# Kernel tuning notes

Hardware: AMD Instinct MI355X
Metric: run time of the kernel (lower is better)

Reference implementation:

```python
import jax, jax.numpy as jnp
import numpy as np
from jax import lax

FILTER_SIZE = 11
SIGMA = 1.5
K1, K2 = 0.01, 0.03
WEIGHTS = jnp.array([0.0448, 0.2856, 0.3001, 0.2363, 0.1333], dtype=jnp.float32)


def _gauss_1d(size, sigma):
    coords = jnp.arange(size, dtype=jnp.float32) - (size - 1) / 2.0
    return jax.nn.softmax(-coords ** 2 / (2.0 * sigma ** 2))


def _gaussian_filter(x, k1d):
    # separable depthwise blur, VALID padding: horizontal then vertical
    C = x.shape[1]
    size = k1d.shape[0]
    kw = jnp.broadcast_to(k1d.reshape(1, 1, 1, size), (C, 1, 1, size))  # OIHW
    kh = jnp.broadcast_to(k1d.reshape(1, 1, size, 1), (C, 1, size, 1))
    dn = ('NCHW', 'OIHW', 'NCHW')
    x = lax.conv_general_dilated(x, kw, (1, 1), 'VALID', dimension_numbers=dn, feature_group_count=C)
    x = lax.conv_general_dilated(x, kh, (1, 1), 'VALID', dimension_numbers=dn, feature_group_count=C)
    return x


def _ssim(x, y, k1d, max_val):
    c1 = (K1 * max_val) ** 2
    c2 = (K2 * max_val) ** 2
    mu1 = _gaussian_filter(x, k1d)
    mu2 = _gaussian_filter(y, k1d)
    mu1_sq, mu2_sq, mu1_mu2 = mu1 ** 2, mu2 ** 2, mu1 * mu2
    sigma1_sq = _gaussian_filter(x * x, k1d) - mu1_sq
    sigma2_sq = _gaussian_filter(y * y, k1d) - mu2_sq
    sigma12 = _gaussian_filter(x * y, k1d) - mu1_mu2
    cs_map = (2 * sigma12 + c2) / (sigma1_sq + sigma2_sq + c2)
    ssim_map = (2 * mu1_mu2 + c1) / (mu1_sq + mu2_sq + c1) * cs_map
    return ssim_map.mean(axis=(-1, -2, -3)), cs_map.mean(axis=(-1, -2, -3))


def _avg_pool2(x):
    # torch avg_pool2d(kernel=2, padding=(H%2, W%2)), count_include_pad=True
    ph, pw = x.shape[-2] % 2, x.shape[-1] % 2
    if ph or pw:
        x = jnp.pad(x, ((0, 0), (0, 0), (ph, ph), (pw, pw)))
    N, C, H, W = x.shape
    return x.reshape(N, C, H // 2, 2, W // 2, 2).mean(axis=(-3, -1))


def setup_inputs() -> dict:
    key = jax.random.key(0)
    k1, k2 = jax.random.split(key)
    shape = (32, 3, 512, 512)
    return {
        'input': jax.random.uniform(k1, shape, dtype=jnp.float32),
        'target': jax.random.uniform(k2, shape, dtype=jnp.float32),
    }


def reference(input, target):
    k1d = _gauss_1d(FILTER_SIZE, SIGMA)
    max_val = target.max() - target.min()  # module default: max_val=None
    levels = WEIGHTS.shape[0]
    x, y = input, target
    mcs = []
    ssim_val = None
    for _ in range(levels):
        ssim_val, cs = _ssim(x, y, k1d, max_val)
        mcs.append(cs)
        x = _avg_pool2(x)
        y = _avg_pool2(y)
    mcs = jnp.stack(mcs, axis=0)  # (levels, N)
    # faithful to original: ssim_val ** w[-1] broadcast inside the product
    ms = jnp.prod(mcs[:-1] ** WEIGHTS[:-1, None] * ssim_val ** WEIGHTS[-1], axis=0)
    return ms.mean()
```

## Files before the change

kernel.cpp:

```cpp
#include <hip/hip_runtime.h>
#include <cmath>

#define FILT 11

typedef float v2f __attribute__((ext_vector_type(2)));

struct GW { float w[FILT]; };

__device__ __forceinline__ unsigned enc_f(float f) {
    unsigned u = __float_as_uint(f);
    return (u & 0x80000000u) ? ~u : (u | 0x80000000u);
}
__device__ __forceinline__ float dec_f(unsigned u) {
    return (u & 0x80000000u) ? __uint_as_float(u & 0x7FFFFFFFu)
                             : __uint_as_float(~u);
}

__global__ void init_acc(unsigned* ws) {
    int t = threadIdx.x;
    if (t == 0) { ws[0] = 0u; ws[1] = 0xFFFFFFFFu; }
    for (int i = 2 + t; i < 512; i += blockDim.x) ws[i] = 0u;
}

__global__ void minmax_kernel(const float4* __restrict__ t, long n4, unsigned* mm) {
    unsigned mx = 0u, mn = 0xFFFFFFFFu;
    long stride = (long)gridDim.x * blockDim.x;
    for (long i = (long)blockIdx.x * blockDim.x + threadIdx.x; i < n4; i += stride) {
        float4 v = t[i];
        unsigned a = enc_f(v.x), b = enc_f(v.y), c = enc_f(v.z), d = enc_f(v.w);
        mx = max(mx, max(max(a, b), max(c, d)));
        mn = min(mn, min(min(a, b), min(c, d)));
    }
    for (int off = 32; off; off >>= 1) {
        mx = max(mx, (unsigned)__shfl_down((int)mx, off));
        mn = min(mn, (unsigned)__shfl_down((int)mn, off));
    }
    __shared__ unsigned smx[4], smn[4];
    int wid = threadIdx.x >> 6, lane = threadIdx.x & 63;
    if (lane == 0) { smx[wid] = mx; smn[wid] = mn; }
    __syncthreads();
    if (threadIdx.x == 0) {
        for (int i = 1; i < 4; i++) { mx = max(mx, smx[i]); mn = min(mn, smn[i]); }
        atomicMax(&mm[0], mx);
        atomicMin(&mm[1], mn);
    }
}

__global__ __launch_bounds__(256) void ssim_stream(
    const float* __restrict__ x, const float* __restrict__ y,
    int H, int W, int NC, int nstrips, int nb, int B,
    const unsigned* __restrict__ mm,
    float* __restrict__ cs_sum, float* __restrict__ ssim_sum, GW gw,
    float* __restrict__ poolx, float* __restrict__ pooly, int do_pool)
{
    __shared__ v2f ring[4][2][80];

    const int wv = threadIdx.x >> 6;
    const int lane = threadIdx.x & 63;
    const int wid = blockIdx.x * 4 + wv;
    const int total = NC * nstrips * nb;
    if (wid >= total) return;

    const int band = wid % nb;
    const int t1 = wid / nb;
    const int strip = t1 % nstrips;
    const int img = t1 / nstrips;
    const int n = img / 3;

    const int Ho = H - (FILT - 1);
    const int Wo = W - (FILT - 1);
    const int a = band * B;
    if (a >= Ho) return;
    const int out_hi = min(a + B, Ho);
    const int bEnd = out_hi + (FILT - 1);

    const int base = strip * 64;
    const float* xp = x + (size_t)img * H * W;
    const float* yp = y + (size_t)img * H * W;
    const int c0 = min(base + lane, W - 1);
    const int c1 = min(base + 64 + min(lane, 9), W - 1);
    const bool colv = (base + lane) < Wo;

    const float mv = dec_f(mm[0]) - dec_f(mm[1]);
    const float c1c = (0.01f * mv) * (0.01f * mv);
    const float c2c = (0.03f * mv) * (0.03f * mv);

    const int Wp = W >> 1;
    size_t orow = (size_t)img * (H >> 1) * Wp + (size_t)(a >> 1) * Wp;
    const int pc = (base >> 1) + lane;
    const bool poolv = (lane < 32) && (pc < Wp);

    v2f* bufE = &ring[wv][0][0];
    v2f* bufO = &ring[wv][1][0];

    v2f acc01[FILT], acc23[FILT];
    float acc4[FILT];
#pragma unroll
    for (int s = 0; s < FILT; s++) {
        acc01[s] = (v2f){0.f, 0.f};
        acc23[s] = (v2f){0.f, 0.f};
        acc4[s] = 0.f;
    }

    float lcs = 0.f, lss = 0.f;

    float ex0, ey0, ex1, ey1, ox0, oy0, ox1, oy1;
    {
        const float* xe = xp + (size_t)a * W;
        const float* ye = yp + (size_t)a * W;
        ex0 = xe[c0]; ey0 = ye[c0]; ex1 = xe[c1]; ey1 = ye[c1];
        ox0 = xe[W + c0]; oy0 = ye[W + c0];
        ox1 = xe[W + c1]; oy1 = ye[W + c1];
    }
    const float* xe = xp + (size_t)(a + 2) * W;
    const float* ye = yp + (size_t)(a + 2) * W;
    const float* xo = xp + (size_t)(a + 3) * W;
    const float* yo = yp + (size_t)(a + 3) * W;

#pragma unroll 1
    for (int r0 = a; r0 < bEnd; r0 += 22) {
#pragma unroll
        for (int p = 0; p < FILT; p++) {
            const int r = r0 + 2 * p;
            if (r < bEnd) {
                const bool hasO = (r + 1 < bEnd);
                const int pe = (2 * p) % FILT;
                const int po = (2 * p + 1) % FILT;

                bufE[lane] = (v2f){ex0, ey0};
                if (lane < 10) bufE[64 + lane] = (v2f){ex1, ey1};
                if (hasO) {
                    bufO[lane] = (v2f){ox0, oy0};
                    if (lane < 10) bufO[64 + lane] = (v2f){ox1, oy1};
                }

                ex0 = xe[c0]; ey0 = ye[c0]; ex1 = xe[c1]; ey1 = ye[c1];
                ox0 = xo[c0]; oy0 = yo[c0]; ox1 = xo[c1]; oy1 = yo[c1];
                {
                    const int adv = (r + 4 < bEnd) ? 2 * W : 0;
                    xe += adv; ye += adv; xo += adv; yo += adv;
                }

                if (do_pool && hasO && poolv) {
                    float4 qe = *(const float4*)&bufE[2 * lane];
                    float4 qo = *(const float4*)&bufO[2 * lane];
                    poolx[orow + pc] = 0.25f * (qe.x + qe.z + qo.x + qo.z);
                    pooly[orow + pc] = 0.25f * (qe.y + qe.w + qo.y + qo.w);
                }
                orow += Wp;

                v2f h01e = (v2f){0.f, 0.f}, h23e = (v2f){0.f, 0.f};
                float h4e = 0.f;
#pragma unroll
                for (int k = 0; k < FILT; k++) {
                    v2f v = bufE[lane + k];
                    float w = gw.w[k];
                    v2f w2 = {w, w};
                    h01e = __builtin_elementwise_fma(w2, v, h01e);
                    v2f sq = v * v;
                    h23e = __builtin_elementwise_fma(w2, sq, h23e);
                    h4e = __builtin_fmaf(w, v.x * v.y, h4e);
                }
#pragma unroll
                for (int k = 0; k < FILT; k++) {
                    const int s = (pe - k + FILT) % FILT;
                    float w = gw.w[k];
                    v2f w2 = {w, w};
                    acc01[s] = __builtin_elementwise_fma(w2, h01e, acc01[s]);
                    acc23[s] = __builtin_elementwise_fma(w2, h23e, acc23[s]);
                    acc4[s] = __builtin_fmaf(w, h4e, acc4[s]);
                }
                const int eE = (pe + 1) % FILT;
                if (r >= a + (FILT - 1) && colv) {
                    float m1 = acc01[eE].x, m2 = acc01[eE].y;
                    float mu11 = m1 * m1, mu22 = m2 * m2, mu12 = m1 * m2;
                    float s1 = acc23[eE].x - mu11;
                    float s2 = acc23[eE].y - mu22;
                    float s12 = acc4[eE] - mu12;
                    float A = 2.f * s12 + c2c, Bv = s1 + s2 + c2c;
                    float Cv = 2.f * mu12 + c1c, Dv = mu11 + mu22 + c1c;
                    float r_ = __builtin_amdgcn_rcpf(Bv * Dv);
                    lcs += A * Dv * r_;
                    lss += Cv * A * r_;
                }
                acc01[eE] = (v2f){0.f, 0.f};
                acc23[eE] = (v2f){0.f, 0.f};
                acc4[eE] = 0.f;

                if (hasO) {
                    v2f h01o = (v2f){0.f, 0.f}, h23o = (v2f){0.f, 0.f};
                    float h4o = 0.f;
#pragma unroll
                    for (int k = 0; k < FILT; k++) {
                        v2f v = bufO[lane + k];
                        float w = gw.w[k];
                        v2f w2 = {w, w};
                        h01o = __builtin_elementwise_fma(w2, v, h01o);
                        v2f sq = v * v;
                        h23o = __builtin_elementwise_fma(w2, sq, h23o);
                        h4o = __builtin_fmaf(w, v.x * v.y, h4o);
                    }
#pragma unroll
                    for (int k = 0; k < FILT; k++) {
                        const int s = (po - k + FILT) % FILT;
                        float w = gw.w[k];
                        v2f w2 = {w, w};
                        acc01[s] = __builtin_elementwise_fma(w2, h01o, acc01[s]);
                        acc23[s] = __builtin_elementwise_fma(w2, h23o, acc23[s]);
                        acc4[s] = __builtin_fmaf(w, h4o, acc4[s]);
                    }
                    const int eO = (po + 1) % FILT;
                    if (r >= a + (FILT - 1) && colv) {
                        float m1 = acc01[eO].x, m2 = acc01[eO].y;
                        float mu11 = m1 * m1, mu22 = m2 * m2, mu12 = m1 * m2;
                        float s1 = acc23[eO].x - mu11;
                        float s2 = acc23[eO].y - mu22;
                        float s12 = acc4[eO] - mu12;
                        float A = 2.f * s12 + c2c, Bv = s1 + s2 + c2c;
                        float Cv = 2.f * mu12 + c1c, Dv = mu11 + mu22 + c1c;
                        float r_ = __builtin_amdgcn_rcpf(Bv * Dv);
                        lcs += A * Dv * r_;
                        lss += Cv * A * r_;
                    }
                    acc01[eO] = (v2f){0.f, 0.f};
                    acc23[eO] = (v2f){0.f, 0.f};
                    acc4[eO] = 0.f;
                }
            }
        }
    }

    for (int off = 32; off; off >>= 1) {
        lcs += __shfl_down(lcs, off);
        lss += __shfl_down(lss, off);
    }
    if (lane == 0) {
        atomicAdd(&cs_sum[n], lcs);
        atomicAdd(&ssim_sum[n], lss);
    }
}

__device__ __forceinline__ void ssim_lds_strip(
    const v2f* tile, int Wt, int Wo, int a, int out_hi, int lane,
    float c1c, float c2c, const GW& gw, float& lcs, float& lss)
{
    const int bEnd = out_hi + (FILT - 1);
    const int tl = min(lane, Wo - 1);
    const bool colv = lane < Wo;

    v2f acc01[FILT], acc23[FILT];
    float acc4[FILT];
#pragma unroll
    for (int s = 0; s < FILT; s++) {
        acc01[s] = (v2f){0.f, 0.f};
        acc23[s] = (v2f){0.f, 0.f};
        acc4[s] = 0.f;
    }

#pragma unroll 1
    for (int r0 = a; r0 < bEnd; r0 += FILT) {
#pragma unroll
        for (int p = 0; p < FILT; p++) {
            const int r = r0 + p;
            if (r < bEnd) {
                const v2f* row = tile + (size_t)r * Wt;
                v2f h01 = (v2f){0.f, 0.f}, h23 = (v2f){0.f, 0.f};
                float h4 = 0.f;
#pragma unroll
                for (int k = 0; k < FILT; k++) {
                    v2f v = row[tl + k];
                    float w = gw.w[k];
                    v2f w2 = {w, w};
                    h01 = __builtin_elementwise_fma(w2, v, h01);
                    v2f sq = v * v;
                    h23 = __builtin_elementwise_fma(w2, sq, h23);
                    h4 = __builtin_fmaf(w, v.x * v.y, h4);
                }
#pragma unroll
                for (int k = 0; k < FILT; k++) {
                    const int s = (p - k + FILT) % FILT;
                    float w = gw.w[k];
                    v2f w2 = {w, w};
                    acc01[s] = __builtin_elementwise_fma(w2, h01, acc01[s]);
                    acc23[s] = __builtin_elementwise_fma(w2, h23, acc23[s]);
                    acc4[s] = __builtin_fmaf(w, h4, acc4[s]);
                }
                const int e = (p + 1) % FILT;
                if (r >= a + (FILT - 1) && colv) {
                    float m1 = acc01[e].x, m2 = acc01[e].y;
                    float mu11 = m1 * m1, mu22 = m2 * m2, mu12 = m1 * m2;
                    float s1 = acc23[e].x - mu11;
                    float s2 = acc23[e].y - mu22;
                    float s12 = acc4[e] - mu12;
                    float A = 2.f * s12 + c2c, Bv = s1 + s2 + c2c;
                    float Cv = 2.f * mu12 + c1c, Dv = mu11 + mu22 + c1c;
                    float r_ = __builtin_amdgcn_rcpf(Bv * Dv);
                    lcs += A * Dv * r_;
                    lss += Cv * A * r_;
                }
                acc01[e] = (v2f){0.f, 0.f};
                acc23[e] = (v2f){0.f, 0.f};
                acc4[e] = 0.f;
            }
        }
    }
}

__global__ __launch_bounds__(1024) void ssim_tail(
    const float* __restrict__ x2, const float* __restrict__ y2,
    const unsigned* __restrict__ mm, float* __restrict__ ws2, GW gw,
    float* __restrict__ outp)
{
    __shared__ v2f ring[16][2][80];
    __shared__ v2f buf3[64 * 64];
    __shared__ v2f buf4[32 * 32];
    __shared__ int isLast;

    const int img = blockIdx.x;
    const int n = img / 3;
    const int wv = threadIdx.x >> 6;
    const int lane = threadIdx.x & 63;

    float* cs2 = ws2 + 2 + 2 * 32;
    float* cs3 = ws2 + 2 + 3 * 32;
    float* cs4 = ws2 + 2 + 4 * 32;
    float* ss2 = ws2 + 2 + 5 * 32 + 2 * 32;
    float* ss3 = ws2 + 2 + 5 * 32 + 3 * 32;
    float* ss4 = ws2 + 2 + 5 * 32 + 4 * 32;

    const float mv = dec_f(mm[0]) - dec_f(mm[1]);
    const float c1c = (0.01f * mv) * (0.01f * mv);
    const float c2c = (0.03f * mv) * (0.03f * mv);

    {
        const int strip = wv >> 3;
        const int band = wv & 7;
        const int H = 128, W = 128, Ho = 118, B = 16;
        const int a = band * B;
        const int out_hi = min(a + B, Ho);
        const int bEnd = out_hi + (FILT - 1);
        const int base = strip * 64;
        const float* xp = x2 + (size_t)img * H * W;
        const float* yp = y2 + (size_t)img * H * W;
        const int c0 = min(base + lane, W - 1);
        const int c1 = min(base + 64 + min(lane, 9), W - 1);
        const bool colv = (base + lane) < Ho;

        v2f* bufA = &ring[wv][0][0];
        v2f* bufB = &ring[wv][1][0];

        v2f acc01[FILT], acc23[FILT];
        float acc4[FILT];
#pragma unroll
        for (int s = 0; s < FILT; s++) {
            acc01[s] = (v2f){0.f, 0.f};
            acc23[s] = (v2f){0.f, 0.f};
            acc4[s] = 0.f;
        }
        float lcs = 0.f, lss = 0.f;

        const float* xr = xp + (size_t)a * W;
        const float* yr = yp + (size_t)a * W;
        float pfx0 = xr[c0], pfy0 = yr[c0];
        float pfx1 = xr[c1], pfy1 = yr[c1];

#pragma unroll 1
        for (int r0 = a; r0 < bEnd; r0 += FILT) {
#pragma unroll
            for (int p = 0; p < FILT; p++) {
                const int r = r0 + p;
                if (r < bEnd) {
                    v2f* bufc = (r & 1) ? bufB : bufA;
                    v2f* bufo = (r & 1) ? bufA : bufB;

                    bufc[lane] = (v2f){pfx0, pfy0};
                    if (lane < 10) bufc[64 + lane] = (v2f){pfx1, pfy1};

                    {
                        const int rn = min(r + 1, bEnd - 1);
                        const float* xn = xp + (size_t)rn * W;
                        const float* yn = yp + (size_t)rn * W;
                        pfx0 = xn[c0]; pfy0 = yn[c0];
                        pfx1 = xn[c1]; pfy1 = yn[c1];
                    }

                    v2f h01 = (v2f){0.f, 0.f}, h23 = (v2f){0.f, 0.f};
                    float h4 = 0.f;
#pragma unroll
                    for (int k = 0; k < FILT; k++) {
                        v2f v = bufc[lane + k];
                        float w = gw.w[k];
                        v2f w2 = {w, w};
                        h01 = __builtin_elementwise_fma(w2, v, h01);
                        v2f sq = v * v;
                        h23 = __builtin_elementwise_fma(w2, sq, h23);
                        h4 = __builtin_fmaf(w, v.x * v.y, h4);
                    }
#pragma unroll
                    for (int k = 0; k < FILT; k++) {
                        const int s = (p - k + FILT) % FILT;
                        float w = gw.w[k];
                        v2f w2 = {w, w};
                        acc01[s] = __builtin_elementwise_fma(w2, h01, acc01[s]);
                        acc23[s] = __builtin_elementwise_fma(w2, h23, acc23[s]);
                        acc4[s] = __builtin_fmaf(w, h4, acc4[s]);
                    }
                    const int e = (p + 1) % FILT;
                    if (r >= a + (FILT - 1) && colv) {
                        float m1 = acc01[e].x, m2 = acc01[e].y;
                        float mu11 = m1 * m1, mu22 = m2 * m2, mu12 = m1 * m2;
                        float s1 = acc23[e].x - mu11;
                        float s2 = acc23[e].y - mu22;
                        float s12 = acc4[e] - mu12;
                        float A = 2.f * s12 + c2c, Bv = s1 + s2 + c2c;
                        float Cv = 2.f * mu12 + c1c, Dv = mu11 + mu22 + c1c;
                        float r_ = __builtin_amdgcn_rcpf(Bv * Dv);
                        lcs += A * Dv * r_;
                        lss += Cv * A * r_;
                    }
                    acc01[e] = (v2f){0.f, 0.f};
                    acc23[e] = (v2f){0.f, 0.f};
                    acc4[e] = 0.f;

                    if ((r & 1) && r > a && lane < 32) {
                        const int pc = (base >> 1) + lane;
                        const int pr = r >> 1;
                        v2f q00 = bufo[2 * lane];
                        v2f q01 = bufo[2 * lane + 1];
                        v2f q10 = bufc[2 * lane];
                        v2f q11 = bufc[2 * lane + 1];
                        buf3[pr * 64 + pc] =
                            (q00 + q01 + q10 + q11) * (v2f){0.25f, 0.25f};
                    }
                }
            }
        }

        for (int off = 32; off; off >>= 1) {
            lcs += __shfl_down(lcs, off);
            lss += __shfl_down(lss, off);
        }
        if (lane == 0) {
            atomicAdd(&cs2[n], lcs);
            atomicAdd(&ss2[n], lss);
        }
    }
    __syncthreads();

    {
        const int pr = threadIdx.x >> 5;
        const int pc = threadIdx.x & 31;
        v2f q = (buf3[(2 * pr) * 64 + 2 * pc] + buf3[(2 * pr) * 64 + 2 * pc + 1] +
                 buf3[(2 * pr + 1) * 64 + 2 * pc] + buf3[(2 * pr + 1) * 64 + 2 * pc + 1]) *
                (v2f){0.25f, 0.25f};
        buf4[pr * 32 + pc] = q;
    }
    __syncthreads();

    {
        float lcs = 0.f, lss = 0.f;
        bool isL3 = (wv < 14);
        if (isL3) {
            const int a = wv * 4;
            ssim_lds_strip(buf3, 64, 54, a, min(a + 4, 54), lane,
                           c1c, c2c, gw, lcs, lss);
        } else {
            const int a = (wv - 14) * 12;
            ssim_lds_strip(buf4, 32, 22, a, min(a + 12, 22), lane,
                           c1c, c2c, gw, lcs, lss);
        }
        for (int off = 32; off; off >>= 1) {
            lcs += __shfl_down(lcs, off);
            lss += __shfl_down(lss, off);
        }
        if (lane == 0) {
            atomicAdd(isL3 ? &cs3[n] : &cs4[n], lcs);
            atomicAdd(isL3 ? &ss3[n] : &ss4[n], lss);
        }
    }

    __syncthreads();
    __threadfence();
    if (threadIdx.x == 0) {
        int old = atomicAdd((int*)(ws2 + 500), 1);
        isLast = (old == (int)gridDim.x - 1);
    }
    __syncthreads();
    if (isLast && threadIdx.x < 64) {
        const float cnt[5] = {3.f * 502 * 502, 3.f * 246 * 246, 3.f * 118 * 118,
                              3.f * 54 * 54, 3.f * 22 * 22};
        const float wts[5] = {0.0448f, 0.2856f, 0.3001f, 0.2363f, 0.1333f};
        int nn = threadIdx.x;
        float ms = 0.f;
        if (nn < 32) {
            float* cs = ws2 + 2;
            float* ss = ws2 + 2 + 5 * 32;
            float ssim = atomicAdd(&ss[4 * 32 + nn], 0.f) / cnt[4];
            float t = powf(ssim, wts[4]);
            ms = 1.f;
            for (int l = 0; l < 4; l++) {
                float cv = atomicAdd(&cs[l * 32 + nn], 0.f) / cnt[l];
                ms *= powf(cv, wts[l]) * t;
            }
        }
        for (int off = 32; off; off >>= 1) ms += __shfl_down(ms, off);
        if (threadIdx.x == 0) outp[0] = ms / 32.f;
    }
}

extern "C" void kernel_launch(void* const* d_in, const int* in_sizes, int n_in,
                              void* d_out, int out_size, void* d_ws, size_t ws_size,
                              hipStream_t stream) {
    const float* x0 = (const float*)d_in[0];
    const float* y0 = (const float*)d_in[1];
    float* out = (float*)d_out;
    float* ws = (float*)d_ws;
    unsigned* mm = (unsigned*)d_ws;
    float* cs_sum = ws + 2;
    float* ssim_sum = ws + 2 + 5 * 32;

    const int N = 32, C = 3, NC = N * C;

    float* wp = ws + 512;
    float* pxw1 = wp; wp += (size_t)NC * 256 * 256;
    float* pyw1 = wp; wp += (size_t)NC * 256 * 256;
    float* pxw2 = wp; wp += (size_t)NC * 128 * 128;
    float* pyw2 = wp; wp += (size_t)NC * 128 * 128;

    GW gw;
    {
        double tmp[FILT], s = 0.0;
        for (int k = 0; k < FILT; k++) {
            double c = (double)k - (FILT - 1) / 2.0;
            tmp[k] = exp(-c * c / (2.0 * 1.5 * 1.5));
            s += tmp[k];
        }
        for (int k = 0; k < FILT; k++) gw.w[k] = (float)(tmp[k] / s);
    }

    init_acc<<<1, 256, 0, stream>>>(mm);
    long n4 = (long)NC * 512 * 512 / 4;
    minmax_kernel<<<2048, 256, 0, stream>>>((const float4*)y0, n4, mm);

    {
        int H = 512, Ho = 502, nstrips = 8, B = 64;
        int nb = (Ho + B - 1) / B;
        int total = NC * nstrips * nb;
        int grid = (total + 3) / 4;
        ssim_stream<<<grid, 256, 0, stream>>>(
            x0, y0, H, H, NC, nstrips, nb, B, mm,
            cs_sum + 0 * 32, ssim_sum + 0 * 32, gw, pxw1, pyw1, 1);
    }
    {
        int H = 256, Ho = 246, nstrips = 4, B = 32;
        int nb = (Ho + B - 1) / B;
        int total = NC * nstrips * nb;
        int grid = (total + 3) / 4;
        ssim_stream<<<grid, 256, 0, stream>>>(
            pxw1, pyw1, H, H, NC, nstrips, nb, B, mm,
            cs_sum + 1 * 32, ssim_sum + 1 * 32, gw, pxw2, pyw2, 1);
    }
    ssim_tail<<<NC, 1024, 0, stream>>>(pxw2, pyw2, mm, ws, gw, out);
}
```

Baseline: 322.0 us.

## Process two adjacent columns per lane in streaming SSIM kernel

```diff
diff --git a/kernel.cpp b/kernel.cpp
--- a/kernel.cpp
+++ b/kernel.cpp
@@ -46,14 +46,14 @@
     }
 }
 
-__global__ __launch_bounds__(256) void ssim_stream(
+__global__ __launch_bounds__(256) void ssim_stream2(
     const float* __restrict__ x, const float* __restrict__ y,
     int H, int W, int NC, int nstrips, int nb, int B,
     const unsigned* __restrict__ mm,
     float* __restrict__ cs_sum, float* __restrict__ ssim_sum, GW gw,
     float* __restrict__ poolx, float* __restrict__ pooly, int do_pool)
 {
-    __shared__ v2f ring[4][2][80];
+    __shared__ v2f ring[4][2][144];
 
     const int wv = threadIdx.x >> 6;
     const int lane = threadIdx.x & 63;
@@ -74,12 +74,13 @@
     const int out_hi = min(a + B, Ho);
     const int bEnd = out_hi + (FILT - 1);
 
-    const int base = strip * 64;
+    const int base = strip * 128;
     const float* xp = x + (size_t)img * H * W;
     const float* yp = y + (size_t)img * H * W;
-    const int c0 = min(base + lane, W - 1);
-    const int c1 = min(base + 64 + min(lane, 9), W - 1);
-    const bool colv = (base + lane) < Wo;
+    const int cA = min(base + 2 * lane, W - 2);
+    const int cH = min(base + 128 + 2 * lane, W - 2);
+    const bool colvA = (base + 2 * lane) < Wo;
+    const bool colvB = (base + 2 * lane + 1) < Wo;
 
     const float mv = dec_f(mm[0]) - dec_f(mm[1]);
     const float c1c = (0.01f * mv) * (0.01f * mv);
@@ -88,29 +89,31 @@
     const int Wp = W >> 1;
     size_t orow = (size_t)img * (H >> 1) * Wp + (size_t)(a >> 1) * Wp;
     const int pc = (base >> 1) + lane;
-    const bool poolv = (lane < 32) && (pc < Wp);
+    const bool poolv = pc < Wp;
 
     v2f* bufE = &ring[wv][0][0];
     v2f* bufO = &ring[wv][1][0];
 
-    v2f acc01[FILT], acc23[FILT];
-    float acc4[FILT];
+    v2f aA01[FILT], aA23[FILT], aB01[FILT], aB23[FILT];
+    float aA4[FILT], aB4[FILT];
 #pragma unroll
     for (int s = 0; s < FILT; s++) {
-        acc01[s] = (v2f){0.f, 0.f};
-        acc23[s] = (v2f){0.f, 0.f};
-        acc4[s] = 0.f;
+        aA01[s] = (v2f){0.f, 0.f}; aA23[s] = (v2f){0.f, 0.f}; aA4[s] = 0.f;
+        aB01[s] = (v2f){0.f, 0.f}; aB23[s] = (v2f){0.f, 0.f}; aB4[s] = 0.f;
     }
 
     float lcs = 0.f, lss = 0.f;
 
-    float ex0, ey0, ex1, ey1, ox0, oy0, ox1, oy1;
+    float2 fxE, fyE, fxO, fyO, hxE, hyE, hxO, hyO;
     {
-        const float* xe = xp + (size_t)a * W;
-        const float* ye = yp + (size_t)a * W;
-        ex0 = xe[c0]; ey0 = ye[c0]; ex1 = xe[c1]; ey1 = ye[c1];
-        ox0 = xe[W + c0]; oy0 = ye[W + c0];
-        ox1 = xe[W + c1]; oy1 = ye[W + c1];
+        const float* x0r = xp + (size_t)a * W;
+        const float* y0r = yp + (size_t)a * W;
+        fxE = *(const float2*)&x0r[cA]; fyE = *(const float2*)&y0r[cA];
+        fxO = *(const float2*)&x0r[W + cA]; fyO = *(const float2*)&y0r[W + cA];
+        if (lane < 5) {
+            hxE = *(const float2*)&x0r[cH]; hyE = *(const float2*)&y0r[cH];
+            hxO = *(const float2*)&x0r[W + cH]; hyO = *(const float2*)&y0r[W + cH];
+        }
     }
     const float* xe = xp + (size_t)(a + 2) * W;
     const float* ye = yp + (size_t)(a + 2) * W;
@@ -123,108 +126,173 @@
         for (int p = 0; p < FILT; p++) {
             const int r = r0 + 2 * p;
             if (r < bEnd) {
-                const bool hasO = (r + 1 < bEnd);
                 const int pe = (2 * p) % FILT;
                 const int po = (2 * p + 1) % FILT;
 
-                bufE[lane] = (v2f){ex0, ey0};
-                if (lane < 10) bufE[64 + lane] = (v2f){ex1, ey1};
-                if (hasO) {
-                    bufO[lane] = (v2f){ox0, oy0};
-                    if (lane < 10) bufO[64 + lane] = (v2f){ox1, oy1};
-                }
-
-                ex0 = xe[c0]; ey0 = ye[c0]; ex1 = xe[c1]; ey1 = ye[c1];
-                ox0 = xo[c0]; oy0 = yo[c0]; ox1 = xo[c1]; oy1 = yo[c1];
+                *(float4*)&bufE[2 * lane] = make_float4(fxE.x, fyE.x, fxE.y, fyE.y);
+                *(float4*)&bufO[2 * lane] = make_float4(fxO.x, fyO.x, fxO.y, fyO.y);
+                if (lane < 5) {
+                    *(float4*)&bufE[128 + 2 * lane] = make_float4(hxE.x, hyE.x, hxE.y, hyE.y);
+                    *(float4*)&bufO[128 + 2 * lane] = make_float4(hxO.x, hyO.x, hxO.y, hyO.y);
+                }
+
+                if (do_pool && poolv) {
+                    poolx[orow + pc] = 0.25f * (fxE.x + fxE.y + fxO.x + fxO.y);
+                    pooly[orow + pc] = 0.25f * (fyE.x + fyE.y + fyO.x + fyO.y);
+                }
+                orow += Wp;
+
+                fxE = *(const float2*)&xe[cA]; fyE = *(const float2*)&ye[cA];
+                fxO = *(const float2*)&xo[cA]; fyO = *(const float2*)&yo[cA];
+                if (lane < 5) {
+                    hxE = *(const float2*)&xe[cH]; hyE = *(const float2*)&ye[cH];
+                    hxO = *(const float2*)&xo[cH]; hyO = *(const float2*)&yo[cH];
+                }
                 {
                     const int adv = (r + 4 < bEnd) ? 2 * W : 0;
                     xe += adv; ye += adv; xo += adv; yo += adv;
                 }
 
-                if (do_pool && hasO && poolv) {
-                    float4 qe = *(const float4*)&bufE[2 * lane];
-                    float4 qo = *(const float4*)&bufO[2 * lane];
-                    poolx[orow + pc] = 0.25f * (qe.x + qe.z + qo.x + qo.z);
-                    pooly[orow + pc] = 0.25f * (qe.y + qe.w + qo.y + qo.w);
-                }
-                orow += Wp;
-
-                v2f h01e = (v2f){0.f, 0.f}, h23e = (v2f){0.f, 0.f};
-                float h4e = 0.f;
-#pragma unroll
-                for (int k = 0; k < FILT; k++) {
-                    v2f v = bufE[lane + k];
-                    float w = gw.w[k];
-                    v2f w2 = {w, w};
-                    h01e = __builtin_elementwise_fma(w2, v, h01e);
-                    v2f sq = v * v;
-                    h23e = __builtin_elementwise_fma(w2, sq, h23e);
-                    h4e = __builtin_fmaf(w, v.x * v.y, h4e);
-                }
-#pragma unroll
-                for (int k = 0; k < FILT; k++) {
-                    const int s = (pe - k + FILT) % FILT;
-                    float w = gw.w[k];
-                    v2f w2 = {w, w};
-                    acc01[s] = __builtin_elementwise_fma(w2, h01e, acc01[s]);
-                    acc23[s] = __builtin_elementwise_fma(w2, h23e, acc23[s]);
-                    acc4[s] = __builtin_fmaf(w, h4e, acc4[s]);
-                }
-                const int eE = (pe + 1) % FILT;
-                if (r >= a + (FILT - 1) && colv) {
-                    float m1 = acc01[eE].x, m2 = acc01[eE].y;
-                    float mu11 = m1 * m1, mu22 = m2 * m2, mu12 = m1 * m2;
-                    float s1 = acc23[eE].x - mu11;
-                    float s2 = acc23[eE].y - mu22;
-                    float s12 = acc4[eE] - mu12;
-                    float A = 2.f * s12 + c2c, Bv = s1 + s2 + c2c;
-                    float Cv = 2.f * mu12 + c1c, Dv = mu11 + mu22 + c1c;
-                    float r_ = __builtin_amdgcn_rcpf(Bv * Dv);
-                    lcs += A * Dv * r_;
-                    lss += Cv * A * r_;
-                }
-                acc01[eE] = (v2f){0.f, 0.f};
-                acc23[eE] = (v2f){0.f, 0.f};
-                acc4[eE] = 0.f;
-
-                if (hasO) {
-                    v2f h01o = (v2f){0.f, 0.f}, h23o = (v2f){0.f, 0.f};
-                    float h4o = 0.f;
+                {
+                    float4 t0 = *(const float4*)&bufE[2 * lane + 0];
+                    float4 t1 = *(const float4*)&bufE[2 * lane + 2];
+                    float4 t2 = *(const float4*)&bufE[2 * lane + 4];
+                    float4 t3 = *(const float4*)&bufE[2 * lane + 6];
+                    float4 t4 = *(const float4*)&bufE[2 * lane + 8];
+                    float4 t5 = *(const float4*)&bufE[2 * lane + 10];
+                    v2f v[12];
+                    v[0] = (v2f){t0.x, t0.y}; v[1] = (v2f){t0.z, t0.w};
+                    v[2] = (v2f){t1.x, t1.y}; v[3] = (v2f){t1.z, t1.w};
+                    v[4] = (v2f){t2.x, t2.y}; v[5] = (v2f){t2.z, t2.w};
+                    v[6] = (v2f){t3.x, t3.y}; v[7] = (v2f){t3.z, t3.w};
+                    v[8] = (v2f){t4.x, t4.y}; v[9] = (v2f){t4.z, t4.w};
+                    v[10] = (v2f){t5.x, t5.y}; v[11] = (v2f){t5.z, t5.w};
+
+                    v2f h01A = (v2f){0.f, 0.f}, h23A = (v2f){0.f, 0.f};
+                    v2f h01B = (v2f){0.f, 0.f}, h23B = (v2f){0.f, 0.f};
+                    float h4A = 0.f, h4B = 0.f;
 #pragma unroll
                     for (int k = 0; k < FILT; k++) {
-                        v2f v = bufO[lane + k];
                         float w = gw.w[k];
                         v2f w2 = {w, w};
-                        h01o = __builtin_elementwise_fma(w2, v, h01o);
-                        v2f sq = v * v;
-                        h23o = __builtin_elementwise_fma(w2, sq, h23o);
-                        h4o = __builtin_fmaf(w, v.x * v.y, h4o);
+                        v2f va = v[k], vb = v[k + 1];
+                        h01A = __builtin_elementwise_fma(w2, va, h01A);
+                        h23A = __builtin_elementwise_fma(w2, va * va, h23A);
+                        h4A = __builtin_fmaf(w, va.x * va.y, h4A);
+                        h01B = __builtin_elementwise_fma(w2, vb, h01B);
+                        h23B = __builtin_elementwise_fma(w2, vb * vb, h23B);
+                        h4B = __builtin_fmaf(w, vb.x * vb.y, h4B);
+                    }
+#pragma unroll
+                    for (int k = 0; k < FILT; k++) {
+                        const int s = (pe - k + FILT) % FILT;
+                        float w = gw.w[k];
+                        v2f w2 = {w, w};
+                        aA01[s] = __builtin_elementwise_fma(w2, h01A, aA01[s]);
+                        aA23[s] = __builtin_elementwise_fma(w2, h23A, aA23[s]);
+                        aA4[s] = __builtin_fmaf(w, h4A, aA4[s]);
+                        aB01[s] = __builtin_elementwise_fma(w2, h01B, aB01[s]);
+                        aB23[s] = __builtin_elementwise_fma(w2, h23B, aB23[s]);
+                        aB4[s] = __builtin_fmaf(w, h4B, aB4[s]);
+                    }
+                    const int e = (pe + 1) % FILT;
+                    if (r >= a + (FILT - 1)) {
+                        if (colvA) {
+                            float m1 = aA01[e].x, m2 = aA01[e].y;
+                            float mu11 = m1 * m1, mu22 = m2 * m2, mu12 = m1 * m2;
+                            float s1 = aA23[e].x - mu11, s2 = aA23[e].y - mu22;
+                            float s12 = aA4[e] - mu12;
+                            float A = 2.f * s12 + c2c, Bv = s1 + s2 + c2c;
+                            float Cv = 2.f * mu12 + c1c, Dv = mu11 + mu22 + c1c;
+                            float r_ = __builtin_amdgcn_rcpf(Bv * Dv);
+                            lcs += A * Dv * r_;
+                            lss += Cv * A * r_;
+                        }
+                        if (colvB) {
+                            float m1 = aB01[e].x, m2 = aB01[e].y;
+                            float mu11 = m1 * m1, mu22 = m2 * m2, mu12 = m1 * m2;
+                            float s1 = aB23[e].x - mu11, s2 = aB23[e].y - mu22;
+                            float s12 = aB4[e] - mu12;
+                            float A = 2.f * s12 + c2c, Bv = s1 + s2 + c2c;
+                            float Cv = 2.f * mu12 + c1c, Dv = mu11 + mu22 + c1c;
+                            float r_ = __builtin_amdgcn_rcpf(Bv * Dv);
+                            lcs += A * Dv * r_;
+                            lss += Cv * A * r_;
+                        }
+                    }
+                    aA01[e] = (v2f){0.f, 0.f}; aA23[e] = (v2f){0.f, 0.f}; aA4[e] = 0.f;
+                    aB01[e] = (v2f){0.f, 0.f}; aB23[e] = (v2f){0.f, 0.f}; aB4[e] = 0.f;
+                }
+
+                {
+                    float4 t0 = *(const float4*)&bufO[2 * lane + 0];
+                    float4 t1 = *(const float4*)&bufO[2 * lane + 2];
+                    float4 t2 = *(const float4*)&bufO[2 * lane + 4];
+                    float4 t3 = *(const float4*)&bufO[2 * lane + 6];
+                    float4 t4 = *(const float4*)&bufO[2 * lane + 8];
+                    float4 t5 = *(const float4*)&bufO[2 * lane + 10];
+                    v2f v[12];
+                    v[0] = (v2f){t0.x, t0.y}; v[1] = (v2f){t0.z, t0.w};
+                    v[2] = (v2f){t1.x, t1.y}; v[3] = (v2f){t1.z, t1.w};
+                    v[4] = (v2f){t2.x, t2.y}; v[5] = (v2f){t2.z, t2.w};
+                    v[6] = (v2f){t3.x, t3.y}; v[7] = (v2f){t3.z, t3.w};
+                    v[8] = (v2f){t4.x, t4.y}; v[9] = (v2f){t4.z, t4.w};
+                    v[10] = (v2f){t5.x, t5.y}; v[11] = (v2f){t5.z, t5.w};
+
+                    v2f h01A = (v2f){0.f, 0.f}, h23A = (v2f){0.f, 0.f};
+                    v2f h01B = (v2f){0.f, 0.f}, h23B = (v2f){0.f, 0.f};
+                    float h4A = 0.f, h4B = 0.f;
+#pragma unroll
+                    for (int k = 0; k < FILT; k++) {
+                        float w = gw.w[k];
+                        v2f w2 = {w, w};
+                        v2f va = v[k], vb = v[k + 1];
+                        h01A = __builtin_elementwise_fma(w2, va, h01A);
+                        h23A = __builtin_elementwise_fma(w2, va * va, h23A);
+                        h4A = __builtin_fmaf(w, va.x * va.y, h4A);
+                        h01B = __builtin_elementwise_fma(w2, vb, h01B);
+                        h23B = __builtin_elementwise_fma(w2, vb * vb, h23B);
+                        h4B = __builtin_fmaf(w, vb.x * vb.y, h4B);
                     }
 #pragma unroll
                     for (int k = 0; k < FILT; k++) {
                         const int s = (po - k + FILT) % FILT;
                         float w = gw.w[k];
                         v2f w2 = {w, w};
-                        acc01[s] = __builtin_elementwise_fma(w2, h01o, acc01[s]);
-                        acc23[s] = __builtin_elementwise_fma(w2, h23o, acc23[s]);
-                        acc4[s] = __builtin_fmaf(w, h4o, acc4[s]);
-                    }
-                    const int eO = (po + 1) % FILT;
-                    if (r >= a + (FILT - 1) && colv) {
-                        float m1 = acc01[eO].x, m2 = acc01[eO].y;
-                        float mu11 = m1 * m1, mu22 = m2 * m2, mu12 = m1 * m2;
-                        float s1 = acc23[eO].x - mu11;
-                        float s2 = acc23[eO].y - mu22;
-                        float s12 = acc4[eO] - mu12;
-                        float A = 2.f * s12 + c2c, Bv = s1 + s2 + c2c;
-                        float Cv = 2.f * mu12 + c1c, Dv = mu11 + mu22 + c1c;
-                        float r_ = __builtin_amdgcn_rcpf(Bv * Dv);
-                        lcs += A * Dv * r_;
-                        lss += Cv * A * r_;
-                    }
-                    acc01[eO] = (v2f){0.f, 0.f};
-                    acc23[eO] = (v2f){0.f, 0.f};
-                    acc4[eO] = 0.f;
+                        aA01[s] = __builtin_elementwise_fma(w2, h01A, aA01[s]);
+                        aA23[s] = __builtin_elementwise_fma(w2, h23A, aA23[s]);
+                        aA4[s] = __builtin_fmaf(w, h4A, aA4[s]);
+                        aB01[s] = __builtin_elementwise_fma(w2, h01B, aB01[s]);
+                        aB23[s] = __builtin_elementwise_fma(w2, h23B, aB23[s]);
+                        aB4[s] = __builtin_fmaf(w, h4B, aB4[s]);
+                    }
+                    const int e = (po + 1) % FILT;
+                    if (r >= a + (FILT - 1)) {
+                        if (colvA) {
+                            float m1 = aA01[e].x, m2 = aA01[e].y;
+                            float mu11 = m1 * m1, mu22 = m2 * m2, mu12 = m1 * m2;
+                            float s1 = aA23[e].x - mu11, s2 = aA23[e].y - mu22;
+                            float s12 = aA4[e] - mu12;
+                            float A = 2.f * s12 + c2c, Bv = s1 + s2 + c2c;
+                            float Cv = 2.f * mu12 + c1c, Dv = mu11 + mu22 + c1c;
+                            float r_ = __builtin_amdgcn_rcpf(Bv * Dv);
+                            lcs += A * Dv * r_;
+                            lss += Cv * A * r_;
+                        }
+                        if (colvB) {
+                            float m1 = aB01[e].x, m2 = aB01[e].y;
+                            float mu11 = m1 * m1, mu22 = m2 * m2, mu12 = m1 * m2;
+                            float s1 = aB23[e].x - mu11, s2 = aB23[e].y - mu22;
+                            float s12 = aB4[e] - mu12;
+                            float A = 2.f * s12 + c2c, Bv = s1 + s2 + c2c;
+                            float Cv = 2.f * mu12 + c1c, Dv = mu11 + mu22 + c1c;
+                            float r_ = __builtin_amdgcn_rcpf(Bv * Dv);
+                            lcs += A * Dv * r_;
+                            lss += Cv * A * r_;
+                        }
+                    }
+                    aA01[e] = (v2f){0.f, 0.f}; aA23[e] = (v2f){0.f, 0.f}; aA4[e] = 0.f;
+                    aB01[e] = (v2f){0.f, 0.f}; aB23[e] = (v2f){0.f, 0.f}; aB4[e] = 0.f;
                 }
             }
         }
@@ -423,13 +491,13 @@
                     acc4[e] = 0.f;
 
                     if ((r & 1) && r > a && lane < 32) {
-                        const int pc = (base >> 1) + lane;
+                        const int pcl = (base >> 1) + lane;
                         const int pr = r >> 1;
                         v2f q00 = bufo[2 * lane];
                         v2f q01 = bufo[2 * lane + 1];
                         v2f q10 = bufc[2 * lane];
                         v2f q11 = bufc[2 * lane + 1];
-                        buf3[pr * 64 + pc] =
+                        buf3[pr * 64 + pcl] =
                             (q00 + q01 + q10 + q11) * (v2f){0.25f, 0.25f};
                     }
                 }
@@ -449,11 +517,11 @@
 
     {
         const int pr = threadIdx.x >> 5;
-        const int pc = threadIdx.x & 31;
-        v2f q = (buf3[(2 * pr) * 64 + 2 * pc] + buf3[(2 * pr) * 64 + 2 * pc + 1] +
-                 buf3[(2 * pr + 1) * 64 + 2 * pc] + buf3[(2 * pr + 1) * 64 + 2 * pc + 1]) *
+        const int pcl = threadIdx.x & 31;
+        v2f q = (buf3[(2 * pr) * 64 + 2 * pcl] + buf3[(2 * pr) * 64 + 2 * pcl + 1] +
+                 buf3[(2 * pr + 1) * 64 + 2 * pcl] + buf3[(2 * pr + 1) * 64 + 2 * pcl + 1]) *
                 (v2f){0.25f, 0.25f};
-        buf4[pr * 32 + pc] = q;
+        buf4[pr * 32 + pcl] = q;
     }
     __syncthreads();
 
@@ -543,20 +611,22 @@
     minmax_kernel<<<2048, 256, 0, stream>>>((const float4*)y0, n4, mm);
 
     {
-        int H = 512, Ho = 502, nstrips = 8, B = 64;
-        int nb = (Ho + B - 1) / B;
+        int H = 512, Ho = 502;
+        int nstrips = (Ho + 127) / 128;
+        int B = 64, nb = (Ho + B - 1) / B;
         int total = NC * nstrips * nb;
         int grid = (total + 3) / 4;
-        ssim_stream<<<grid, 256, 0, stream>>>(
+        ssim_stream2<<<grid, 256, 0, stream>>>(
             x0, y0, H, H, NC, nstrips, nb, B, mm,
             cs_sum + 0 * 32, ssim_sum + 0 * 32, gw, pxw1, pyw1, 1);
     }
     {
-        int H = 256, Ho = 246, nstrips = 4, B = 32;
-        int nb = (Ho + B - 1) / B;
+        int H = 256, Ho = 246;
+        int nstrips = (Ho + 127) / 128;
+        int B = 32, nb = (Ho + B - 1) / B;
         int total = NC * nstrips * nb;
         int grid = (total + 3) / 4;
-        ssim_stream<<<grid, 256, 0, stream>>>(
+        ssim_stream2<<<grid, 256, 0, stream>>>(
             pxw1, pyw1, H, H, NC, nstrips, nb, B, mm,
             cs_sum + 1 * 32, ssim_sum + 1 * 32, gw, pxw2, pyw2, 1);
     }
```

New measurement: 291.1 us. 1.11x faster.
